# Optimization experiments

Hardware: AMD Instinct MI355X
Metric: run time of the kernel (lower is better)

## Reference

```python
import jax, jax.numpy as jnp
import numpy as np

# 3x3 laplacian stencil, OIHW
LAP = jnp.array([-1, -1, -1, -1, 8, -1, -1, -1, -1], dtype=jnp.float32).reshape(1, 1, 3, 3)
THR = 0.1
SMOOTH = 1.0


def _lap_conv(x, stride):
    # x: [B,1,H,W]
    return jax.lax.conv_general_dilated(
        x, LAP, window_strides=(stride, stride), padding=((1, 1), (1, 1)),
        dimension_numbers=('NCHW', 'OIHW', 'NCHW'))


def _nearest_up(x, H, W):
    # PyTorch 'nearest': src_idx = floor(dst_idx * in/out)
    h, w = x.shape[2], x.shape[3]
    ri = (jnp.arange(H) * h) // H
    ci = (jnp.arange(W) * w) // W
    return x[:, :, ri][:, :, :, ci]


def _thresh(x):
    return jnp.where(x > THR, 1.0, 0.0).astype(x.dtype)


def setup_inputs() -> dict:
    key = jax.random.key(0)
    k1, k2 = jax.random.split(key)
    B, H, W = 16, 1024, 1024
    boundary_logits = jax.random.normal(k1, (B, 1, H, W), dtype=jnp.float32)
    gtmasks = (jax.random.uniform(k2, (B, H, W)) > 0.5).astype(jnp.float32)
    fuse_kernel = jnp.array([0.6, 0.3, 0.1], dtype=jnp.float32).reshape(1, 3, 1, 1)
    return {"boundary_logits": boundary_logits, "gtmasks": gtmasks, "fuse_kernel": fuse_kernel}


def reference(boundary_logits, gtmasks, fuse_kernel):
    g = gtmasks[:, None, :, :].astype(jnp.float32)  # [B,1,H,W]
    bt = _thresh(jnp.maximum(_lap_conv(g, 1), 0.0))  # full res
    H, W = bt.shape[2], bt.shape[3]
    bt2 = _thresh(_nearest_up(jnp.maximum(_lap_conv(g, 2), 0.0), H, W))
    bt4 = _thresh(_nearest_up(jnp.maximum(_lap_conv(g, 4), 0.0), H, W))
    # (x8 branch in original is computed but unused in the output)
    pyr = jnp.concatenate([bt, bt2, bt4], axis=1)  # [B,3,H,W]
    fused = jnp.einsum('bchw,c->bhw', pyr, fuse_kernel.reshape(3))[:, None]  # 1x1 fuse conv
    target = _thresh(fused)  # [B,1,H,W]

    x = boundary_logits
    # stable BCE with logits, mean reduction
    bce_loss = jnp.mean(jnp.maximum(x, 0.0) - x * target + jnp.log1p(jnp.exp(-jnp.abs(x))))

    p = jax.nn.sigmoid(x)
    n = p.shape[0]
    pf = p.reshape(n, -1)
    tf = target.reshape(n, -1)
    inter = jnp.sum(pf * tf, axis=1)
    dice_loss = jnp.mean(1.0 - (2.0 * inter + SMOOTH) / (jnp.sum(pf, 1) + jnp.sum(tf, 1) + SMOOTH))
    return bce_loss, dice_loss
```

## Files before the change

kernel.cpp:

```cpp
#include <hip/hip_runtime.h>

#define IMG_H 1024
#define IMG_W 1024
#define NIMG  16
#define NPIX  16777216.0f
#define NBLK  4096
#define LOG2E 1.44269504088896340736f
#define LN2   0.69314718055994530942f

#ifndef __has_builtin
#define __has_builtin(x) 0
#endif

__device__ __forceinline__ void stage16(const float* src, float* dstLds, int lane) {
#if __has_builtin(__builtin_amdgcn_global_load_lds)
    __builtin_amdgcn_global_load_lds(
        (const __attribute__((address_space(1))) void*)src,
        (__attribute__((address_space(3))) void*)dstLds,
        16, 0, 0);
#else
    *reinterpret_cast<float4*>(dstLds + (lane << 2)) =
        *reinterpret_cast<const float4*>(src);
#endif
}


__global__ __launch_bounds__(256, 6) void dal_main(
    const float* __restrict__ xlogits,
    const float* __restrict__ gmask,
    const float* __restrict__ fuse,
    float4* __restrict__ ws4)
{
    __shared__ float lds[6 * 1024];

    const int bid = blockIdx.x;
    const int b   = (bid & 7) * (NBLK / 8) + (bid >> 3);

    const int img  = b >> 8;
    const int r0   = (b & 255) << 2;
    const int tid  = (int)threadIdx.x;
    const int wid  = tid >> 6;
    const int lane = tid & 63;
    const int j0   = tid * 4;

    const float w0 = fuse[0], w1 = fuse[1], w2 = fuse[2];

    const size_t ibase = (size_t)img * (IMG_H * IMG_W);
    const float* gi = gmask + ibase;
    const float* xi = xlogits + ibase;

    #pragma unroll
    for (int t = 0; t < 6; ++t) {
        int r  = r0 - 1 + t;
        int rc = r < 0 ? 0 : (r > IMG_H - 1 ? IMG_H - 1 : r);
        stage16(gi + (size_t)rc * IMG_W + j0, &lds[t * 1024 + (wid << 8)], lane);
    }

    float4 xv[4];
    const float* xr = xi + (size_t)r0 * IMG_W + j0;
    #pragma unroll
    for (int r = 0; r < 4; ++r)
        xv[r] = *reinterpret_cast<const float4*>(xr + (size_t)r * IMG_W);

    __syncthreads();

    const bool hasL = (j0 > 0);
    const bool hasR = (j0 + 4 < IMG_W);
    const int  jl   = hasL ? j0 - 1 : 0;
    const int  jr   = hasR ? j0 + 4 : IMG_W - 1;

    auto fold = [&](int t, float* rm, float* cvo) {
        const float* Lr = &lds[t * 1024];
        float4 v   = *reinterpret_cast<const float4*>(Lr + j0);
        float  lf0 = Lr[jl];
        float  rg0 = Lr[jr];
        float  lf  = hasL ? lf0 : 0.f;
        float  rg  = hasR ? rg0 : 0.f;
        rm[0] = fminf(lf,  fminf(v.x, v.y));
        rm[1] = fminf(v.x, fminf(v.y, v.z));
        rm[2] = fminf(v.y, fminf(v.z, v.w));
        rm[3] = fminf(v.z, fminf(v.w, rg));
        cvo[0] = v.x; cvo[1] = v.y; cvo[2] = v.z; cvo[3] = v.w;
    };

    float rm[6][4], cv[4][4], tmp[4];
    fold(0, rm[0], tmp);
    fold(1, rm[1], cv[0]);
    fold(2, rm[2], cv[1]);
    fold(3, rm[3], cv[2]);
    fold(4, rm[4], cv[3]);
    fold(5, rm[5], tmp);
    if (r0 == 0)         { rm[0][0] = rm[0][1] = rm[0][2] = rm[0][3] = 0.f; }
    if (r0 == IMG_H - 4) { rm[5][0] = rm[5][1] = rm[5][2] = rm[5][3] = 0.f; }

    float bt[4][4];
    #pragma unroll
    for (int r = 0; r < 4; ++r)
        #pragma unroll
        for (int k = 0; k < 4; ++k) {
            float cm = fminf(rm[r][k], fminf(rm[r + 1][k], rm[r + 2][k]));
            bt[r][k] = (cv[r][k] > 0.5f && cm < 0.5f) ? 1.f : 0.f;
        }

    const float wb4 = w2 * bt[0][0];
    float base2[2][2];
    base2[0][0] = fmaf(w1, bt[0][0], wb4);
    base2[0][1] = fmaf(w1, bt[0][2], wb4);
    base2[1][0] = fmaf(w1, bt[2][0], wb4);
    base2[1][1] = fmaf(w1, bt[2][2], wb4);

    float l2[2]  = {0.f, 0.f}, xt[2] = {0.f, 0.f};
    float itr[2] = {0.f, 0.f}, sp[2] = {0.f, 0.f};
    int st = 0;

    auto px = [&](float x, float btv, float b2v, int a) {
        float f = fmaf(w0, btv, b2v);
        bool  c = f > 0.1f;
        st += (int)__popcll(__ballot(c));
        float u   = __builtin_amdgcn_exp2f(x * LOG2E);
        float opu = 1.f + u;
        float p   = u * __builtin_amdgcn_rcpf(opu);
        l2[a]  += __builtin_amdgcn_logf(opu);
        sp[a]  += p;
        xt[a]  += c ? x : 0.f;
        itr[a] += c ? p : 0.f;
    };

    #pragma unroll
    for (int r = 0; r < 4; ++r) {
        const float bA = base2[r >> 1][0];
        const float bB = base2[r >> 1][1];
        px(xv[r].x, bt[r][0], bA, r & 1);
        px(xv[r].y, bt[r][1], bA, r & 1);
        px(xv[r].z, bt[r][2], bB, r & 1);
        px(xv[r].w, bt[r][3], bB, r & 1);
    }

    float bce   = fmaf(LN2, l2[0] + l2[1], -(xt[0] + xt[1]));
    float inter = itr[0] + itr[1];
    float sump  = sp[0] + sp[1];

    #pragma unroll
    for (int off = 32; off > 0; off >>= 1) {
        bce   += __shfl_down(bce, off);
        inter += __shfl_down(inter, off);
        sump  += __shfl_down(sump, off);
    }
    __syncthreads();
    if (lane == 0) {
        lds[wid]      = bce;
        lds[4 + wid]  = inter;
        lds[8 + wid]  = sump;
        lds[12 + wid] = (float)st;
    }
    __syncthreads();
    if (tid == 0) {
        float4 o;
        o.x = (lds[0]  + lds[1])  + (lds[2]  + lds[3]);
        o.y = (lds[4]  + lds[5])  + (lds[6]  + lds[7]);
        o.z = (lds[8]  + lds[9])  + (lds[10] + lds[11]);
        o.w = (lds[12] + lds[13]) + (lds[14] + lds[15]);
        ws4[b] = o;
    }
}

__global__ __launch_bounds__(1024) void dal_finalize(
    const float4* __restrict__ ws4, float* __restrict__ out)
{
    const int t    = (int)threadIdx.x;
    const int wv   = t >> 6;
    const int lane = t & 63;
    const int i0   = t * 4;

    float4 a = ws4[i0];
    float4 b = ws4[i0 + 1];
    float4 c = ws4[i0 + 2];
    float4 d = ws4[i0 + 3];
    float bce   = (a.x + b.x) + (c.x + d.x);
    float inter = (a.y + b.y) + (c.y + d.y);
    float sump  = (a.z + b.z) + (c.z + d.z);
    float sumt  = (a.w + b.w) + (c.w + d.w);

    #pragma unroll
    for (int off = 32; off > 0; off >>= 1) {
        bce   += __shfl_down(bce, off);
        inter += __shfl_down(inter, off);
        sump  += __shfl_down(sump, off);
        sumt  += __shfl_down(sumt, off);
    }

    __shared__ float sb[16], sd[16];
    if (lane == 0) {
        sb[wv] = bce;
        sd[wv] = 1.f - (2.f * inter + 1.f) / (sump + sumt + 1.f);
    }
    __syncthreads();
    if (t == 0) {
        float tb = 0.f, td = 0.f;
        #pragma unroll
        for (int i = 0; i < NIMG; ++i) { tb += sb[i]; td += sd[i]; }
        out[0] = tb / NPIX;
        out[1] = td / (float)NIMG;
    }
}

extern "C" void kernel_launch(void* const* d_in, const int* in_sizes, int n_in,
                              void* d_out, int out_size, void* d_ws, size_t ws_size,
                              hipStream_t stream)
{
    const float* x    = (const float*)d_in[0];
    const float* g    = (const float*)d_in[1];
    const float* fuse = (const float*)d_in[2];
    float* out = (float*)d_out;
    float4* ws4 = (float4*)d_ws;

    dal_main<<<NBLK, 256, 0, stream>>>(x, g, fuse, ws4);
    dal_finalize<<<1, 1024, 0, stream>>>(ws4, out);
}
```

Baseline: 29.60 us.

## Make each wave self-contained with private LDS halo and drop block barriers

Each wavefront now stages its own 256-column slice of the six mask rows into a private LDS region, with single-float halo columns loaded via 4-byte global_load_lds. It replaces __syncthreads with a wave-local vmcnt wait. The cross-wave partial-sum reduction in LDS is removed: each wave writes its own float4 partial to the workspace, and the finalize kernel sums four times as many entries. This removes block-level barriers and halo reads that cross waves, at the cost of extra halo loads, slightly more LDS, a larger workspace write, and no fallback path when the LDS-load builtin is unavailable.

Result: slower. 36.05 us (+21.8%).

```diff
diff --git a/kernel.cpp b/kernel.cpp
--- a/kernel.cpp
+++ b/kernel.cpp
@@ -12,15 +12,18 @@
 #define __has_builtin(x) 0
 #endif
 
-__device__ __forceinline__ void stage16(const float* src, float* dstLds, int lane) {
+__device__ __forceinline__ void stage16(const float* src, float* dstLds) {
 #if __has_builtin(__builtin_amdgcn_global_load_lds)
     __builtin_amdgcn_global_load_lds(
         (const __attribute__((address_space(1))) void*)src,
-        (__attribute__((address_space(3))) void*)dstLds,
-        16, 0, 0);
-#else
-    *reinterpret_cast<float4*>(dstLds + (lane << 2)) =
-        *reinterpret_cast<const float4*>(src);
+        (__attribute__((address_space(3))) void*)dstLds, 16, 0, 0);
+#endif
+}
+__device__ __forceinline__ void stage4(const float* src, float* dstLds) {
+#if __has_builtin(__builtin_amdgcn_global_load_lds)
+    __builtin_amdgcn_global_load_lds(
+        (const __attribute__((address_space(1))) void*)src,
+        (__attribute__((address_space(3))) void*)dstLds, 4, 0, 0);
 #endif
 }
 
@@ -31,17 +34,18 @@
     const float* __restrict__ fuse,
     float4* __restrict__ ws4)
 {
-    __shared__ float lds[6 * 1024];
+    __shared__ float lds[4 * 1600];
 
     const int bid = blockIdx.x;
     const int b   = (bid & 7) * (NBLK / 8) + (bid >> 3);
 
-    const int img  = b >> 8;
-    const int r0   = (b & 255) << 2;
-    const int tid  = (int)threadIdx.x;
-    const int wid  = tid >> 6;
-    const int lane = tid & 63;
-    const int j0   = tid * 4;
+    const int img    = b >> 8;
+    const int r0     = (b & 255) << 2;
+    const int tid    = (int)threadIdx.x;
+    const int wid    = tid >> 6;
+    const int lane   = tid & 63;
+    const int wstart = wid << 8;
+    const int jg     = wstart + (lane << 2);
 
     const float w0 = fuse[0], w1 = fuse[1], w2 = fuse[2];
 
@@ -49,33 +53,46 @@
     const float* gi = gmask + ibase;
     const float* xi = xlogits + ibase;
 
+    float* wlds = &lds[wid * 1600];
+
     #pragma unroll
     for (int t = 0; t < 6; ++t) {
         int r  = r0 - 1 + t;
         int rc = r < 0 ? 0 : (r > IMG_H - 1 ? IMG_H - 1 : r);
-        stage16(gi + (size_t)rc * IMG_W + j0, &lds[t * 1024 + (wid << 8)], lane);
+        stage16(gi + (size_t)rc * IMG_W + jg, wlds + 64 + t * 256);
+    }
+    {
+        int t6 = (lane < 6) ? lane : ((lane < 12) ? lane - 6 : 1);
+        int rh = r0 - 1 + t6;
+        rh = rh < 0 ? 0 : (rh > IMG_H - 1 ? IMG_H - 1 : rh);
+        int ch = wstart;
+        ch = (lane < 12) ? ((wstart + 256 < IMG_W) ? wstart + 256 : IMG_W - 1) : ch;
+        ch = (lane < 6)  ? ((wstart > 0) ? wstart - 1 : 0)                    : ch;
+        stage4(gi + (size_t)rh * IMG_W + ch, wlds);
     }
 
     float4 xv[4];
-    const float* xr = xi + (size_t)r0 * IMG_W + j0;
+    const float* xr = xi + (size_t)r0 * IMG_W + jg;
     #pragma unroll
     for (int r = 0; r < 4; ++r)
         xv[r] = *reinterpret_cast<const float4*>(xr + (size_t)r * IMG_W);
 
-    __syncthreads();
-
-    const bool hasL = (j0 > 0);
-    const bool hasR = (j0 + 4 < IMG_W);
-    const int  jl   = hasL ? j0 - 1 : 0;
-    const int  jr   = hasR ? j0 + 4 : IMG_W - 1;
+    asm volatile("s_waitcnt vmcnt(0)" ::: "memory");
+    __builtin_amdgcn_sched_barrier(0);
+
+    const bool hasL = (wstart > 0);
+    const bool hasR = (wstart + 256 < IMG_W);
+    const int  bl   = lane << 2;
 
     auto fold = [&](int t, float* rm, float* cvo) {
-        const float* Lr = &lds[t * 1024];
-        float4 v   = *reinterpret_cast<const float4*>(Lr + j0);
-        float  lf0 = Lr[jl];
-        float  rg0 = Lr[jr];
-        float  lf  = hasL ? lf0 : 0.f;
-        float  rg  = hasR ? rg0 : 0.f;
+        const float* Lr = wlds + 64 + t * 256;
+        float4 v = *reinterpret_cast<const float4*>(Lr + bl);
+        int offL = (lane == 0)  ? t       : (64 + t * 256 + bl - 1);
+        int offR = (lane == 63) ? (6 + t) : (64 + t * 256 + bl + 4);
+        float lraw = wlds[offL];
+        float rraw = wlds[offR];
+        float lf = (lane == 0  && !hasL) ? 0.f : lraw;
+        float rg = (lane == 63 && !hasR) ? 0.f : rraw;
         rm[0] = fminf(lf,  fminf(v.x, v.y));
         rm[1] = fminf(v.x, fminf(v.y, v.z));
         rm[2] = fminf(v.y, fminf(v.z, v.w));
@@ -146,21 +163,9 @@
         inter += __shfl_down(inter, off);
         sump  += __shfl_down(sump, off);
     }
-    __syncthreads();
     if (lane == 0) {
-        lds[wid]      = bce;
-        lds[4 + wid]  = inter;
-        lds[8 + wid]  = sump;
-        lds[12 + wid] = (float)st;
-    }
-    __syncthreads();
-    if (tid == 0) {
-        float4 o;
-        o.x = (lds[0]  + lds[1])  + (lds[2]  + lds[3]);
-        o.y = (lds[4]  + lds[5])  + (lds[6]  + lds[7]);
-        o.z = (lds[8]  + lds[9])  + (lds[10] + lds[11]);
-        o.w = (lds[12] + lds[13]) + (lds[14] + lds[15]);
-        ws4[b] = o;
+        float4 o; o.x = bce; o.y = inter; o.z = sump; o.w = (float)st;
+        ws4[(b << 2) | wid] = o;
     }
 }
 
@@ -170,16 +175,14 @@
     const int t    = (int)threadIdx.x;
     const int wv   = t >> 6;
     const int lane = t & 63;
-    const int i0   = t * 4;
-
-    float4 a = ws4[i0];
-    float4 b = ws4[i0 + 1];
-    float4 c = ws4[i0 + 2];
-    float4 d = ws4[i0 + 3];
-    float bce   = (a.x + b.x) + (c.x + d.x);
-    float inter = (a.y + b.y) + (c.y + d.y);
-    float sump  = (a.z + b.z) + (c.z + d.z);
-    float sumt  = (a.w + b.w) + (c.w + d.w);
+    const int i0   = t * 16;
+
+    float bce = 0.f, inter = 0.f, sump = 0.f, sumt = 0.f;
+    #pragma unroll
+    for (int i = 0; i < 16; ++i) {
+        float4 a = ws4[i0 + i];
+        bce += a.x; inter += a.y; sump += a.z; sumt += a.w;
+    }
 
     #pragma unroll
     for (int off = 32; off > 0; off >>= 1) {
```
